# Kernel tuning notes

Measured on AMD Instinct MI355X. Metric: run time of the kernel, lower is better.

## Reference

```python
import jax, jax.numpy as jnp
import numpy as np
from jax import lax

B, S, H = 1, 2048, 1024
NH, NKV, HD = 16, 4, 64        # heads, kv heads, head_dim = H // NH
I = 3584                        # intermediate size
E, TOPK = 8, 2                  # experts, top-k routing
EPS = 1e-5
THETA = 1e6


def setup_inputs() -> dict:
    key = jax.random.key(0)
    ks = jax.random.split(key, 12)
    sc = 0.02
    return {
        "hidden_states": jax.random.normal(ks[0], (B, S, H), jnp.float32),
        "position_ids": jnp.broadcast_to(jnp.arange(S, dtype=jnp.int32), (B, S)),
        "wq": jax.random.normal(ks[1], (H, NH * HD), jnp.float32) * sc,
        "wk": jax.random.normal(ks[2], (H, NKV * HD), jnp.float32) * sc,
        "wv": jax.random.normal(ks[3], (H, NKV * HD), jnp.float32) * sc,
        "wo": jax.random.normal(ks[4], (NH * HD, H), jnp.float32) * sc,
        "input_norm_w": jnp.ones((H,), jnp.float32),
        "post_norm_w": jnp.ones((H,), jnp.float32),
        "gate_w": jax.random.normal(ks[5], (H, E), jnp.float32) * sc,
        "w1": jax.random.normal(ks[6], (E, H, I), jnp.float32) * sc,
        "w3": jax.random.normal(ks[7], (E, H, I), jnp.float32) * sc,
        "w2": jax.random.normal(ks[8], (E, I, H), jnp.float32) * sc,
    }


def _rmsnorm(x, w):
    var = jnp.mean(jnp.square(x), axis=-1, keepdims=True)
    return x * lax.rsqrt(var + EPS) * w


def _rope(q, k, position_ids):
    # q: [B,S,NH,HD], k: [B,S,NKV,HD]
    inv_freq = 1.0 / (THETA ** (jnp.arange(0, HD, 2, dtype=jnp.float32) / HD))
    freqs = position_ids.astype(jnp.float32)[..., None] * inv_freq  # [B,S,HD/2]
    emb = jnp.concatenate([freqs, freqs], axis=-1)                  # [B,S,HD]
    cos = jnp.cos(emb)[:, :, None, :]
    sin = jnp.sin(emb)[:, :, None, :]

    def rot_half(x):
        x1, x2 = jnp.split(x, 2, axis=-1)
        return jnp.concatenate([-x2, x1], axis=-1)

    return q * cos + rot_half(q) * sin, k * cos + rot_half(k) * sin


def _attention(x, position_ids, wq, wk, wv, wo):
    b, s, _ = x.shape
    q = (x @ wq).reshape(b, s, NH, HD)
    k = (x @ wk).reshape(b, s, NKV, HD)
    v = (x @ wv).reshape(b, s, NKV, HD)
    q, k = _rope(q, k, position_ids)
    groups = NH // NKV
    k = jnp.repeat(k, groups, axis=2)  # [B,S,NH,HD]
    v = jnp.repeat(v, groups, axis=2)
    scale = HD ** -0.5
    scores = jnp.einsum("bqhd,bkhd->bhqk", q, k) * scale
    causal = jnp.tril(jnp.ones((s, s), dtype=bool))
    scores = jnp.where(causal[None, None], scores, jnp.finfo(scores.dtype).min)
    probs = jax.nn.softmax(scores, axis=-1)
    out = jnp.einsum("bhqk,bkhd->bqhd", probs, v).reshape(b, s, NH * HD)
    return out @ wo


def _moe(x, gate_w, w1, w3, w2):
    b, s, h = x.shape
    xt = x.reshape(b * s, h)
    logits = xt @ gate_w                      # [T,E]
    probs = jax.nn.softmax(logits, axis=-1)
    top_w, top_i = lax.top_k(probs, TOPK)     # [T,K]
    top_w = top_w / jnp.sum(top_w, axis=-1, keepdims=True)
    out = jnp.zeros_like(xt)
    for e in range(E):
        we = jnp.sum(jnp.where(top_i == e, top_w, 0.0), axis=-1)   # [T]
        h_e = jax.nn.silu(xt @ w1[e]) * (xt @ w3[e])               # [T,I]
        out = out + we[:, None] * (h_e @ w2[e])
    return out.reshape(b, s, h), logits


def reference(hidden_states, position_ids, wq, wk, wv, wo,
              input_norm_w, post_norm_w, gate_w, w1, w3, w2):
    # MixtralDecoderLayer: norm -> GQA attn -> residual -> norm -> MoE -> residual
    attn_out = _attention(_rmsnorm(hidden_states, input_norm_w),
                          position_ids, wq, wk, wv, wo)
    h = hidden_states + attn_out
    moe_out, _router_logits = _moe(_rmsnorm(h, post_norm_w), gate_w, w1, w3, w2)
    return h + moe_out
```

## Files before the change

kernel.cpp:

```cpp
#include <hip/hip_runtime.h>
#include <math.h>


typedef unsigned short u16;
typedef unsigned int u32;
typedef __attribute__((ext_vector_type(8))) short s16x8;
typedef __attribute__((ext_vector_type(8))) _Float16 f16x8;
typedef __attribute__((ext_vector_type(4))) float f32x4;

#define S_LEN 2048
#define HDIM  1024
#define NHEAD 16
#define NKVH  4
#define HD    64
#define ISZ   3584
#define NEXP  8
#define NSLOT 4096
#define EPS_F 1e-5f
#define NEG_INF -1e30f
#define LOG2E 1.44269504f

__device__ __forceinline__ float bf2f(u16 u) {
    union { u32 i; float f; } c; c.i = ((u32)u) << 16; return c.f;
}
__device__ __forceinline__ u16 f2bf(float f) {
    union { float f; u32 i; } c; c.f = f;
    u32 r = (c.i + 0x7fffu + ((c.i >> 16) & 1u)) >> 16;
    return (u16)r;
}
__device__ __forceinline__ u16 f2h_bits(float f) {
    union { _Float16 h; u16 u; } c; c.h = (_Float16)f; return c.u;
}
__device__ __forceinline__ void async16(const u16* g, u16* l) {
    __builtin_amdgcn_global_load_lds(
        (const __attribute__((address_space(1))) void*)g,
        (__attribute__((address_space(3))) void*)l, 16, 0, 0);
}

__global__ void k_zero_ints(int* __restrict__ p, int n) {
    int i = blockIdx.x * blockDim.x + threadIdx.x;
    if (i < n) p[i] = 0;
}

__global__ __launch_bounds__(256)
void k_rmsnorm_bf(const float* __restrict__ x, const float* __restrict__ w,
                  u16* __restrict__ out) {
    int t = blockIdx.x;
    int tid = threadIdx.x;
    float4 v = ((const float4*)(x + (size_t)t * HDIM))[tid];
    float ss = v.x * v.x + v.y * v.y + v.z * v.z + v.w * v.w;
#pragma unroll
    for (int off = 32; off >= 1; off >>= 1) ss += __shfl_xor(ss, off, 64);
    __shared__ float red[4];
    if ((tid & 63) == 0) red[tid >> 6] = ss;
    __syncthreads();
    float tot = red[0] + red[1] + red[2] + red[3];
    float rstd = rsqrtf(tot * (1.0f / HDIM) + EPS_F);
    float4 wv = ((const float4*)w)[tid];
    uint2 pk;
    pk.x = (u32)f2bf(v.x * rstd * wv.x) | ((u32)f2bf(v.y * rstd * wv.y) << 16);
    pk.y = (u32)f2bf(v.z * rstd * wv.z) | ((u32)f2bf(v.w * rstd * wv.w) << 16);
    ((uint2*)(out + (size_t)t * HDIM))[tid] = pk;
}

__global__ __launch_bounds__(256)
void k_cvt_t(const float* __restrict__ src, u16* __restrict__ dst,
             int R, int C, long long srcZ, long long dstZ) {
    const int z = blockIdx.z;
    src += (size_t)z * srcZ;
    dst += (size_t)z * dstZ;
    const int lane = threadIdx.x & 63, w = threadIdx.x >> 6;
    const int c = blockIdx.x * 64 + lane;
    const int r0 = blockIdx.y * 128 + w * 32;
    float v[32];
#pragma unroll
    for (int i = 0; i < 32; i++) v[i] = src[(size_t)(r0 + i) * C + c];
#pragma unroll
    for (int g = 0; g < 4; g++) {
        uint4 pk;
        pk.x = (u32)f2bf(v[g * 8 + 0]) | ((u32)f2bf(v[g * 8 + 1]) << 16);
        pk.y = (u32)f2bf(v[g * 8 + 2]) | ((u32)f2bf(v[g * 8 + 3]) << 16);
        pk.z = (u32)f2bf(v[g * 8 + 4]) | ((u32)f2bf(v[g * 8 + 5]) << 16);
        pk.w = (u32)f2bf(v[g * 8 + 6]) | ((u32)f2bf(v[g * 8 + 7]) << 16);
        *(uint4*)(&dst[(size_t)c * R + r0 + g * 8]) = pk;
    }
}

__device__ __forceinline__ void stage32(const u16* __restrict__ A,
                                        const u16* __restrict__ Bt, int K,
                                        int rowA0, int rowAmax, int n0, int kc,
                                        u16* buf, int wid, int sr, int sc) {
#pragma unroll
    for (int t = 0; t < 2; t++) {
        int row = wid * 32 + t * 16 + sr;
        int ck = (sc ^ (row & 3)) << 3;
        int ra = rowA0 + row;
        if (ra > rowAmax) ra = rowAmax;
        u16* ldsA = buf + (wid * 32 + t * 16) * 32;
        async16(A + (size_t)ra * K + kc + ck, ldsA);
        async16(Bt + (size_t)(n0 + row) * K + kc + ck, ldsA + 4096);
    }
}

__device__ __forceinline__ void stage32_w13(const u16* __restrict__ A,
                                            const u16* __restrict__ B1,
                                            const u16* __restrict__ B3, int K,
                                            int rowA0, int rowAmax, int n0,
                                            int kc, u16* buf, int wid, int sr,
                                            int sc) {
#pragma unroll
    for (int t = 0; t < 2; t++) {
        int row = wid * 32 + t * 16 + sr;
        int ck = (sc ^ (row & 3)) << 3;
        int ra = rowA0 + row;
        if (ra > rowAmax) ra = rowAmax;
        u16* ldsA = buf + (wid * 32 + t * 16) * 32;
        async16(A + (size_t)ra * K + kc + ck, ldsA);
        async16(B1 + (size_t)(n0 + row) * K + kc + ck, ldsA + 4096);
        async16(B3 + (size_t)(n0 + row) * K + kc + ck, ldsA + 8192);
    }
}

__device__ __forceinline__ void gemm128_dbuf(
    const u16* __restrict__ A, const u16* __restrict__ Bt, int K,
    int kbeg, int kend, int rowA0, int rowAmax, int n0,
    u16* lds, f32x4 acc[4][4]) {
    const int tid = threadIdx.x;
    const int lane = tid & 63, wid = tid >> 6;
    const int sr = lane >> 2, sc = lane & 3;
    const int ln = lane & 15, q = lane >> 4;
    const int wm = wid >> 1, wn = wid & 1;
    stage32(A, Bt, K, rowA0, rowAmax, n0, kbeg, lds, wid, sr, sc);
    int pp = 0;
    for (int kc = kbeg; kc < kend; kc += 32) {
        u16* cur = lds + pp * 8192;
        u16* nxt = lds + (pp ^ 1) * 8192;
        pp ^= 1;
        __syncthreads();
        if (kc + 32 < kend)
            stage32(A, Bt, K, rowA0, rowAmax, n0, kc + 32, nxt, wid, sr, sc);
        s16x8 af[4], bfv[4];
#pragma unroll
        for (int i = 0; i < 4; i++) {
            int ar = wm * 64 + i * 16 + ln;
            af[i] = *(const s16x8*)(cur + ar * 32 + ((q ^ (ar & 3)) << 3));
            int br = wn * 64 + i * 16 + ln;
            bfv[i] = *(const s16x8*)(cur + 4096 + br * 32 + ((q ^ (br & 3)) << 3));
        }
#pragma unroll
        for (int i = 0; i < 4; i++)
#pragma unroll
            for (int j = 0; j < 4; j++)
                acc[i][j] = __builtin_amdgcn_mfma_f32_16x16x32_bf16(
                    af[i], bfv[j], acc[i][j], 0, 0, 0);
    }
}

__global__ __launch_bounds__(256, 2)
void k_gemm_bt(const u16* __restrict__ A, const u16* __restrict__ Bt,
               int M, int N, int K, int mode,
               float* __restrict__ F0, float* __restrict__ F1,
               const float* __restrict__ RES, u16* __restrict__ O16) {
    __shared__ u16 lds[16384];
    const int m0 = blockIdx.y * 128, n0 = blockIdx.x * 128;
    f32x4 acc[4][4];
#pragma unroll
    for (int i = 0; i < 4; i++)
#pragma unroll
        for (int j = 0; j < 4; j++) acc[i][j] = (f32x4){0.f, 0.f, 0.f, 0.f};
    gemm128_dbuf(A, Bt, K, 0, K, m0, M - 1, n0, lds, acc);
    const int lane = threadIdx.x & 63, wid = threadIdx.x >> 6;
    const int ln = lane & 15, q = lane >> 4, wm = wid >> 1, wn = wid & 1;
#pragma unroll
    for (int i = 0; i < 4; i++) {
#pragma unroll
        for (int r = 0; r < 4; r++) {
            int m = m0 + wm * 64 + i * 16 + q * 4 + r;
#pragma unroll
            for (int j = 0; j < 4; j++) {
                int n = n0 + wn * 64 + j * 16 + ln;
                float v = acc[i][j][r];
                if (mode == 0) {
                    F0[(size_t)m * N + n] = v;
                } else if (mode == 1) {
                    O16[(size_t)m * N + n] = f2bf(v);
                } else if (mode == 2) {
                    F0[(size_t)m * N + n] = v + RES[(size_t)m * N + n];
                } else {
                    if (n < 1024)       F0[(size_t)m * 1024 + n] = v;
                    else if (n < 1280)  F1[(size_t)m * 256 + (n - 1024)] = v;
                    else                O16[(size_t)m * 256 + (n - 1280)] = f2h_bits(v);
                }
            }
        }
    }
}

__global__ __launch_bounds__(256, 2)
void k_moe_w13(const u16* __restrict__ Xg, const u16* __restrict__ W1T,
               const u16* __restrict__ W3T, u16* __restrict__ He,
               const int* __restrict__ offs) {
    const int bid = blockIdx.x;
    const int xcd = bid & 7;
    const int r_ = bid >> 3;
    const int mb = r_ & 15;
    const int gslot = r_ >> 4;
    const int gid = gslot * 8 + xcd;
    const int e = gid / 28;
    const int nb = gid - e * 28;
    const int base = offs[e], cnt = offs[e + 1] - base;
    const int m0 = mb * 128;
    if (m0 >= cnt) return;
    __shared__ u16 lds[24576];
    const u16* B1 = W1T + (size_t)e * ISZ * HDIM;
    const u16* B3 = W3T + (size_t)e * ISZ * HDIM;
    const int n0 = nb * 128;
    f32x4 acc1[4][4], acc3[4][4];
#pragma unroll
    for (int i = 0; i < 4; i++)
#pragma unroll
        for (int j = 0; j < 4; j++) {
            acc1[i][j] = (f32x4){0.f, 0.f, 0.f, 0.f};
            acc3[i][j] = (f32x4){0.f, 0.f, 0.f, 0.f};
        }
    const int tid = threadIdx.x;
    const int lane = tid & 63, wid = tid >> 6;
    const int sr = lane >> 2, sc = lane & 3;
    const int ln = lane & 15, q = lane >> 4;
    const int wm = wid >> 1, wn = wid & 1;
    const int rowA0 = base + m0;
    stage32_w13(Xg, B1, B3, HDIM, rowA0, NSLOT - 1, n0, 0, lds, wid, sr, sc);
    int pp = 0;
    for (int kc = 0; kc < HDIM; kc += 32) {
        u16* cur = lds + pp * 12288;
        u16* nxt = lds + (pp ^ 1) * 12288;
        pp ^= 1;
        __syncthreads();
        if (kc + 32 < HDIM)
            stage32_w13(Xg, B1, B3, HDIM, rowA0, NSLOT - 1, n0, kc + 32, nxt,
                        wid, sr, sc);
        s16x8 af[4], b1f[4], b3f[4];
#pragma unroll
        for (int i = 0; i < 4; i++) {
            int ar = wm * 64 + i * 16 + ln;
            af[i] = *(const s16x8*)(cur + ar * 32 + ((q ^ (ar & 3)) << 3));
            int br = wn * 64 + i * 16 + ln;
            int bo = br * 32 + ((q ^ (br & 3)) << 3);
            b1f[i] = *(const s16x8*)(cur + 4096 + bo);
            b3f[i] = *(const s16x8*)(cur + 8192 + bo);
        }
#pragma unroll
        for (int i = 0; i < 4; i++)
#pragma unroll
            for (int j = 0; j < 4; j++) {
                acc1[i][j] = __builtin_amdgcn_mfma_f32_16x16x32_bf16(
                    af[i], b1f[j], acc1[i][j], 0, 0, 0);
                acc3[i][j] = __builtin_amdgcn_mfma_f32_16x16x32_bf16(
                    af[i], b3f[j], acc3[i][j], 0, 0, 0);
            }
    }
#pragma unroll
    for (int i = 0; i < 4; i++) {
#pragma unroll
        for (int r = 0; r < 4; r++) {
            int mloc = wm * 64 + i * 16 + q * 4 + r;
            if (m0 + mloc >= cnt) continue;
            size_t row = (size_t)(base + m0 + mloc);
#pragma unroll
            for (int j = 0; j < 4; j++) {
                int n = n0 + wn * 64 + j * 16 + ln;
                float v1 = acc1[i][j][r];
                float v3 = acc3[i][j][r];
                float s = v1 / (1.0f + expf(-v1));
                He[row * ISZ + n] = f2bf(s * v3);
            }
        }
    }
}

__global__ __launch_bounds__(256, 2)
void k_moe_w2(const u16* __restrict__ He, const u16* __restrict__ W2T,
              float* __restrict__ OA, float* __restrict__ OB,
              const int* __restrict__ offs) {
    const int z = blockIdx.z;
    const int e = z & 7, half = z >> 3;
    const int base = offs[e], cnt = offs[e + 1] - base;
    const int m0 = blockIdx.y * 128;
    if (m0 >= cnt) return;
    __shared__ u16 lds[16384];
    const u16* Bt = W2T + (size_t)e * HDIM * ISZ;
    const int n0 = blockIdx.x * 128;
    f32x4 acc[4][4];
#pragma unroll
    for (int i = 0; i < 4; i++)
#pragma unroll
        for (int j = 0; j < 4; j++) acc[i][j] = (f32x4){0.f, 0.f, 0.f, 0.f};
    gemm128_dbuf(He, Bt, ISZ, half * (ISZ / 2), (half + 1) * (ISZ / 2),
                 base + m0, NSLOT - 1, n0, lds, acc);
    float* F0 = half ? OB : OA;
    const int lane = threadIdx.x & 63, wid = threadIdx.x >> 6;
    const int ln = lane & 15, q = lane >> 4, wm = wid >> 1, wn = wid & 1;
#pragma unroll
    for (int i = 0; i < 4; i++) {
#pragma unroll
        for (int r = 0; r < 4; r++) {
            int mloc = wm * 64 + i * 16 + q * 4 + r;
            if (m0 + mloc >= cnt) continue;
            size_t row = (size_t)(base + m0 + mloc);
#pragma unroll
            for (int j = 0; j < 4; j++) {
                int n = n0 + wn * 64 + j * 16 + ln;
                F0[row * HDIM + n] = acc[i][j][r];
            }
        }
    }
}

__global__ __launch_bounds__(256)
void k_rope_cvt(const float* __restrict__ q, const float* __restrict__ k,
                const int* __restrict__ pos, u16* __restrict__ qb2,
                u16* __restrict__ kb2) {
    int id = blockIdx.x * blockDim.x + threadIdx.x;
    int d = id & 31;
    int hh = (id >> 5) % (NHEAD + NKVH);
    int s = id / ((NHEAD + NKVH) * 32);
    float p = (float)pos[s];
    float inv = exp2f(-((float)(2 * d) / (float)HD) * log2f(1.0e6f));
    float ang = p * inv;
    float c = cosf(ang), sn = sinf(ang);
    const float* sp; u16* dp;
    if (hh < NHEAD) {
        sp = q + (size_t)s * (NHEAD * HD) + hh * HD;
        dp = qb2 + (size_t)s * (NHEAD * HD) + hh * HD;
    } else {
        sp = k + (size_t)s * (NKVH * HD) + (hh - NHEAD) * HD;
        dp = kb2 + (size_t)s * (NKVH * HD) + (hh - NHEAD) * HD;
    }
    float x1 = sp[d], x2 = sp[d + 32];
    dp[d]      = f2h_bits(x1 * c - x2 * sn);
    dp[d + 32] = f2h_bits(x2 * c + x1 * sn);
}

__global__ __launch_bounds__(256)
void k_attn_mfma(const u16* __restrict__ qb, const u16* __restrict__ kb,
                 const u16* __restrict__ vb, u16* __restrict__ ob) {
    __shared__ u16 Qs[64 * 64];
    __shared__ u16 Ks[64 * 64];
    __shared__ u16 Vt[64 * 64];
    __shared__ u16 Ps[64 * 64];
    const int qt = blockIdx.x, h = blockIdx.y, kvh = h >> 2;
    const int tid = threadIdx.x, lane = tid & 63, w = tid >> 6;
    const int ln = lane & 15, quad = lane >> 4;

#pragma unroll
    for (int p = 0; p < 2; p++) {
        int r = p * 32 + (tid >> 3), c = tid & 7;
        uint4 v = *(const uint4*)(qb + (size_t)(qt * 64 + r) * (NHEAD * HD) +
                                  h * HD + c * 8);
        *(uint4*)&Qs[r * 64 + ((c ^ (r & 7)) << 3)] = v;
    }

    float m_[4], l_[4];
    f32x4 Oa[4];
#pragma unroll
    for (int r = 0; r < 4; r++) { m_[r] = NEG_INF; l_[r] = 0.0f; }
#pragma unroll
    for (int nt = 0; nt < 4; nt++) Oa[nt] = (f32x4){0.f, 0.f, 0.f, 0.f};

    for (int kt = 0; kt <= qt; kt++) {
        __syncthreads();
#pragma unroll
        for (int p = 0; p < 2; p++) {
            int r = p * 32 + (tid >> 3), c = tid & 7;
            uint4 v = *(const uint4*)(kb + (size_t)(kt * 64 + r) * (NKVH * HD) +
                                      kvh * HD + c * 8);
            *(uint4*)&Ks[r * 64 + ((c ^ (r & 7)) << 3)] = v;
        }
        {
            int s = tid & 63;
#pragma unroll
            for (int half = 0; half < 2; half++) {
                int d0 = w * 16 + half * 8;
                uint4 v = *(const uint4*)(vb + (size_t)(kt * 64 + s) * (NKVH * HD) +
                                          kvh * HD + d0);
                u16 a[8];
                a[0] = (u16)(v.x & 0xffff); a[1] = (u16)(v.x >> 16);
                a[2] = (u16)(v.y & 0xffff); a[3] = (u16)(v.y >> 16);
                a[4] = (u16)(v.z & 0xffff); a[5] = (u16)(v.z >> 16);
                a[6] = (u16)(v.w & 0xffff); a[7] = (u16)(v.w >> 16);
#pragma unroll
                for (int j = 0; j < 8; j++) {
                    int d = d0 + j;
                    Vt[d * 64 + (((s >> 3) ^ (d & 7)) << 3) + (s & 7)] = a[j];
                }
            }
        }
        __syncthreads();

        f32x4 sc[4];
#pragma unroll
        for (int nt = 0; nt < 4; nt++) sc[nt] = (f32x4){0.f, 0.f, 0.f, 0.f};
#pragma unroll
        for (int ks = 0; ks < 2; ks++) {
            int arow = 16 * w + ln;
            f16x8 af = *(const f16x8*)&Qs[arow * 64 +
                                          (((ks * 4 + quad) ^ (arow & 7)) << 3)];
#pragma unroll
            for (int nt = 0; nt < 4; nt++) {
                int brow = nt * 16 + ln;
                f16x8 bf = *(const f16x8*)&Ks[brow * 64 +
                                              (((ks * 4 + quad) ^ (brow & 7)) << 3)];
                sc[nt] = __builtin_amdgcn_mfma_f32_16x16x32_f16(af, bf, sc[nt],
                                                                0, 0, 0);
            }
        }

        const bool diag = (kt == qt);
        float mt[4];
#pragma unroll
        for (int r = 0; r < 4; r++) {
            int qrow = quad * 4 + r + 16 * w;
#pragma unroll
            for (int nt = 0; nt < 4; nt++) {
                float s = sc[nt][r] * 0.125f;
                if (diag && (nt * 16 + ln) > qrow) s = NEG_INF;
                sc[nt][r] = s;
            }
            mt[r] = fmaxf(fmaxf(sc[0][r], sc[1][r]), fmaxf(sc[2][r], sc[3][r]));
        }
#pragma unroll
        for (int off = 8; off >= 1; off >>= 1)
#pragma unroll
            for (int r = 0; r < 4; r++)
                mt[r] = fmaxf(mt[r], __shfl_xor(mt[r], off, 64));

        float rs[4];
#pragma unroll
        for (int r = 0; r < 4; r++) {
            float mn = fmaxf(m_[r], mt[r]);
            float al = exp2f((m_[r] - mn) * LOG2E);
            m_[r] = mn;
            float acc0 = 0.0f;
#pragma unroll
            for (int nt = 0; nt < 4; nt++) {
                float pv = exp2f((sc[nt][r] - mn) * LOG2E);
                sc[nt][r] = pv;
                acc0 += pv;
            }
            rs[r] = acc0;
            l_[r] *= al;
#pragma unroll
            for (int nt = 0; nt < 4; nt++) Oa[nt][r] *= al;
        }
#pragma unroll
        for (int off = 8; off >= 1; off >>= 1)
#pragma unroll
            for (int r = 0; r < 4; r++) rs[r] += __shfl_xor(rs[r], off, 64);
#pragma unroll
        for (int r = 0; r < 4; r++) l_[r] += rs[r];

#pragma unroll
        for (int r = 0; r < 4; r++) {
            int row = 16 * w + quad * 4 + r;
#pragma unroll
            for (int nt = 0; nt < 4; nt++) {
                int ch = nt * 2 + (ln >> 3);
                Ps[row * 64 + ((ch ^ (row & 7)) << 3) + (ln & 7)] =
                    f2h_bits(sc[nt][r]);
            }
        }
        __syncthreads();

#pragma unroll
        for (int ks = 0; ks < 2; ks++) {
            int arow = 16 * w + ln;
            f16x8 pf = *(const f16x8*)&Ps[arow * 64 +
                                          (((ks * 4 + quad) ^ (arow & 7)) << 3)];
#pragma unroll
            for (int nt = 0; nt < 4; nt++) {
                int vrow = nt * 16 + ln;
                f16x8 vf = *(const f16x8*)&Vt[vrow * 64 +
                                              (((ks * 4 + quad) ^ (vrow & 7)) << 3)];
                Oa[nt] = __builtin_amdgcn_mfma_f32_16x16x32_f16(pf, vf, Oa[nt],
                                                                0, 0, 0);
            }
        }
    }

#pragma unroll
    for (int r = 0; r < 4; r++) {
        float inv = 1.0f / l_[r];
        int sg = qt * 64 + 16 * w + quad * 4 + r;
#pragma unroll
        for (int nt = 0; nt < 4; nt++) {
            int d = nt * 16 + ln;
            ob[(size_t)sg * HDIM + h * HD + d] = f2bf(Oa[nt][r] * inv);
        }
    }
}

__global__ __launch_bounds__(64)
void k_gate(const float* __restrict__ Hst, const float* __restrict__ PW,
            const float* __restrict__ GW, int* __restrict__ cnt,
            int* __restrict__ top_i, float* __restrict__ top_w) {
    int t = blockIdx.x;
    int lane = threadIdx.x;
    const float* hrow = Hst + (size_t)t * HDIM;
    float ss = 0.0f;
    float acc[NEXP] = {};
    for (int hh = lane; hh < HDIM; hh += 64) {
        float hv = hrow[hh];
        ss += hv * hv;
        float xw = hv * PW[hh];
        const float* g = GW + (size_t)hh * NEXP;
#pragma unroll
        for (int e = 0; e < NEXP; e++) acc[e] += xw * g[e];
    }
#pragma unroll
    for (int off = 32; off >= 1; off >>= 1) {
        ss += __shfl_xor(ss, off, 64);
#pragma unroll
        for (int e = 0; e < NEXP; e++) acc[e] += __shfl_xor(acc[e], off, 64);
    }
    if (lane == 0) {
        float rstd = rsqrtf(ss * (1.0f / HDIM) + EPS_F);
        int e0 = 0;
        for (int e = 1; e < NEXP; e++) if (acc[e] > acc[e0]) e0 = e;
        int e1 = (e0 == 0) ? 1 : 0;
        for (int e = 0; e < NEXP; e++)
            if (e != e0 && acc[e] > acc[e1]) e1 = e;
        float w0 = 1.0f / (1.0f + expf((acc[e1] - acc[e0]) * rstd));
        top_i[t * 2 + 0] = e0; top_i[t * 2 + 1] = e1;
        top_w[t * 2 + 0] = w0; top_w[t * 2 + 1] = 1.0f - w0;
        atomicAdd(&cnt[e0], 1);
        atomicAdd(&cnt[e1], 1);
    }
}

__global__ void k_prefix(const int* __restrict__ cnt, int* __restrict__ offs,
                         int* __restrict__ cur) {
    if (blockIdx.x == 0 && threadIdx.x == 0) {
        int a = 0;
        for (int e = 0; e < NEXP; e++) { offs[e] = a; cur[e] = a; a += cnt[e]; }
        offs[NEXP] = a;
    }
}

__global__ __launch_bounds__(256)
void k_fill(const int* __restrict__ top_i, int* __restrict__ cur,
            int* __restrict__ idxg, int* __restrict__ slot) {
    int t = blockIdx.x * blockDim.x + threadIdx.x;
    if (t >= S_LEN) return;
#pragma unroll
    for (int kk = 0; kk < 2; kk++) {
        int e = top_i[t * 2 + kk];
        int p = atomicAdd(&cur[e], 1);
        idxg[p] = t;
        slot[t * 2 + kk] = p;
    }
}

__global__ __launch_bounds__(256)
void k_gather(const u16* __restrict__ xnb, const int* __restrict__ idxg,
              u16* __restrict__ Xg) {
    int p = blockIdx.x;
    int t = idxg[p];
    const uint2* s = (const uint2*)(xnb + (size_t)t * HDIM);
    uint2* d = (uint2*)(Xg + (size_t)p * HDIM);
    d[threadIdx.x] = s[threadIdx.x];
}

__global__ __launch_bounds__(256)
void k_combine2(const float* __restrict__ OA, const float* __restrict__ OB,
                const int* __restrict__ slot, const float* __restrict__ top_w,
                float* __restrict__ out) {
    int t = blockIdx.x, tid = threadIdx.x;
    int s0 = slot[t * 2], s1 = slot[t * 2 + 1];
    float w0 = top_w[t * 2], w1 = top_w[t * 2 + 1];
    float4 a0 = ((const float4*)(OA + (size_t)s0 * HDIM))[tid];
    float4 b0 = ((const float4*)(OB + (size_t)s0 * HDIM))[tid];
    float4 a1 = ((const float4*)(OA + (size_t)s1 * HDIM))[tid];
    float4 b1 = ((const float4*)(OB + (size_t)s1 * HDIM))[tid];
    float4* o = (float4*)(out + (size_t)t * HDIM);
    float4 c = o[tid];
    c.x += w0 * (a0.x + b0.x) + w1 * (a1.x + b1.x);
    c.y += w0 * (a0.y + b0.y) + w1 * (a1.y + b1.y);
    c.z += w0 * (a0.z + b0.z) + w1 * (a1.z + b1.z);
    c.w += w0 * (a0.w + b0.w) + w1 * (a1.w + b1.w);
    o[tid] = c;
}

extern "C" void kernel_launch(void* const* d_in, const int* in_sizes, int n_in,
                              void* d_out, int out_size, void* d_ws,
                              size_t ws_size, hipStream_t stream) {
    (void)in_sizes; (void)n_in; (void)out_size; (void)ws_size;
    const float* hidden = (const float*)d_in[0];
    const int*   pos    = (const int*)d_in[1];
    const float* wq     = (const float*)d_in[2];
    const float* wk     = (const float*)d_in[3];
    const float* wv     = (const float*)d_in[4];
    const float* wo     = (const float*)d_in[5];
    const float* innw   = (const float*)d_in[6];
    const float* postnw = (const float*)d_in[7];
    const float* gatew  = (const float*)d_in[8];
    const float* w1     = (const float*)d_in[9];
    const float* w3     = (const float*)d_in[10];
    const float* w2     = (const float*)d_in[11];
    float* out = (float*)d_out;

    u16* w1t  = (u16*)d_ws;
    u16* w3t  = w1t + (size_t)NEXP * ISZ * HDIM;
    u16* w2t  = w3t + (size_t)NEXP * ISZ * HDIM;
    u16* qkvt = w2t + (size_t)NEXP * ISZ * HDIM;
    u16* wot  = qkvt + (size_t)1536 * HDIM;
    u16* xnb  = wot + (size_t)HDIM * HDIM;
    float* qbuf = (float*)(xnb + (size_t)S_LEN * HDIM);
    float* kbuf = qbuf + (size_t)S_LEN * HDIM;
    u16* vb16   = (u16*)(kbuf + (size_t)S_LEN * NKVH * HD);
    u16* qb2    = vb16 + (size_t)S_LEN * NKVH * HD;
    u16* kb2    = qb2 + (size_t)S_LEN * HDIM;
    u16* attnb  = kb2 + (size_t)S_LEN * NKVH * HD;
    float* oexpA = qbuf;
    u16* Xg  = attnb + (size_t)S_LEN * HDIM;
    u16* hg3 = Xg + (size_t)NSLOT * HDIM;
    u16* he  = hg3 + (size_t)NSLOT * ISZ;
    float* oexpB = (float*)(he + (size_t)NSLOT * ISZ);
    int* ib  = (int*)(oexpB + (size_t)NSLOT * HDIM);
    int*   cnt   = ib;
    int*   offs  = ib + 16;
    int*   cur   = ib + 32;
    int*   top_i = ib + 64;
    int*   slot  = ib + 64 + 4096;
    int*   idxg  = ib + 64 + 8192;
    float* top_w = (float*)(ib + 64 + 12288);

    const long long HI = (long long)HDIM * ISZ;

    k_zero_ints<<<1, 64, 0, stream>>>(cnt, 64);
    k_rmsnorm_bf<<<S_LEN, 256, 0, stream>>>(hidden, innw, xnb);

    k_cvt_t<<<dim3(16, 8, 1), 256, 0, stream>>>(wq, qkvt, 1024, 1024, 0, 0);
    k_cvt_t<<<dim3(4, 8, 1), 256, 0, stream>>>(wk, qkvt + (size_t)1024 * 1024, 1024, 256, 0, 0);
    k_cvt_t<<<dim3(4, 8, 1), 256, 0, stream>>>(wv, qkvt + (size_t)1280 * 1024, 1024, 256, 0, 0);
    k_cvt_t<<<dim3(16, 8, 1), 256, 0, stream>>>(wo, wot, 1024, 1024, 0, 0);
    k_cvt_t<<<dim3(56, 8, NEXP), 256, 0, stream>>>(w1, w1t, 1024, 3584, HI, HI);
    k_cvt_t<<<dim3(56, 8, NEXP), 256, 0, stream>>>(w3, w3t, 1024, 3584, HI, HI);
    k_cvt_t<<<dim3(16, 28, NEXP), 256, 0, stream>>>(w2, w2t, 3584, 1024, HI, HI);

    k_gemm_bt<<<dim3(12, 16), 256, 0, stream>>>(xnb, qkvt, 2048, 1536, 1024, 3,
                                                qbuf, kbuf, nullptr, vb16);
    k_rope_cvt<<<(S_LEN * (NHEAD + NKVH) * 32) / 256, 256, 0, stream>>>(
        qbuf, kbuf, pos, qb2, kb2);
    k_attn_mfma<<<dim3(32, 16), 256, 0, stream>>>(qb2, kb2, vb16, attnb);
    k_gemm_bt<<<dim3(8, 16), 256, 0, stream>>>(attnb, wot, 2048, 1024, 1024, 2,
                                               out, nullptr, hidden, nullptr);
    k_rmsnorm_bf<<<S_LEN, 256, 0, stream>>>(out, postnw, xnb);
    k_gate<<<S_LEN, 64, 0, stream>>>(out, postnw, gatew, cnt, top_i, top_w);
    k_prefix<<<1, 1, 0, stream>>>(cnt, offs, cur);
    k_fill<<<S_LEN / 256, 256, 0, stream>>>(top_i, cur, idxg, slot);
    k_gather<<<NSLOT, 256, 0, stream>>>(xnb, idxg, Xg);

    k_moe_w13<<<dim3(28 * 16 * NEXP), 256, 0, stream>>>(Xg, w1t, w3t, he, offs);
    k_moe_w2<<<dim3(8, 16, 16), 256, 0, stream>>>(he, w2t, oexpA, oexpB, offs);
    k_combine2<<<S_LEN, 256, 0, stream>>>(oexpA, oexpB, slot, top_w, out);
}
```

Before: 883.4 us.

## Use persistent work-list scheduling for MoE expert GEMMs with 512-thread w13 blocks

k_prefix now writes a compact list of the (expert, m-block) tiles that actually exist. Both MoE GEMM kernels become persistent grid-stride loops over that list, so blocks are no longer launched only to exit early on empty tiles. k_moe_w13 moves to 512 threads (8 waves, each owning a 64x32 sub-tile) with a smaller per-wave accumulator, and occupancy targets are raised. In exchange it drops the previous XCD-aware block ordering and adds per-tile loop overhead and extra barriers.

```diff
diff --git a/kernel.cpp b/kernel.cpp
--- a/kernel.cpp
+++ b/kernel.cpp
@@ -102,23 +102,19 @@
     }
 }
 
-__device__ __forceinline__ void stage32_w13(const u16* __restrict__ A,
-                                            const u16* __restrict__ B1,
-                                            const u16* __restrict__ B3, int K,
-                                            int rowA0, int rowAmax, int n0,
-                                            int kc, u16* buf, int wid, int sr,
-                                            int sc) {
-#pragma unroll
-    for (int t = 0; t < 2; t++) {
-        int row = wid * 32 + t * 16 + sr;
-        int ck = (sc ^ (row & 3)) << 3;
-        int ra = rowA0 + row;
-        if (ra > rowAmax) ra = rowAmax;
-        u16* ldsA = buf + (wid * 32 + t * 16) * 32;
-        async16(A + (size_t)ra * K + kc + ck, ldsA);
-        async16(B1 + (size_t)(n0 + row) * K + kc + ck, ldsA + 4096);
-        async16(B3 + (size_t)(n0 + row) * K + kc + ck, ldsA + 8192);
-    }
+__device__ __forceinline__ void stage_w13(const u16* __restrict__ A,
+                                          const u16* __restrict__ B1,
+                                          const u16* __restrict__ B3,
+                                          int rowA0, int n0, int kc,
+                                          u16* buf, int wid, int sr, int sc) {
+    int row = wid * 16 + sr;
+    int ck = (sc ^ (row & 3)) << 3;
+    int ra = rowA0 + row;
+    if (ra > NSLOT - 1) ra = NSLOT - 1;
+    u16* dst = buf + (wid * 16) * 32;
+    async16(A  + (size_t)ra * HDIM + kc + ck, dst);
+    async16(B1 + (size_t)(n0 + row) * HDIM + kc + ck, dst + 4096);
+    async16(B3 + (size_t)(n0 + row) * HDIM + kc + ck, dst + 8192);
 }
 
 __device__ __forceinline__ void gemm128_dbuf(
@@ -196,121 +192,127 @@
     }
 }
 
-__global__ __launch_bounds__(256, 2)
+__global__ __launch_bounds__(512, 4)
 void k_moe_w13(const u16* __restrict__ Xg, const u16* __restrict__ W1T,
                const u16* __restrict__ W3T, u16* __restrict__ He,
-               const int* __restrict__ offs) {
-    const int bid = blockIdx.x;
-    const int xcd = bid & 7;
-    const int r_ = bid >> 3;
-    const int mb = r_ & 15;
-    const int gslot = r_ >> 4;
-    const int gid = gslot * 8 + xcd;
-    const int e = gid / 28;
-    const int nb = gid - e * 28;
-    const int base = offs[e], cnt = offs[e + 1] - base;
-    const int m0 = mb * 128;
-    if (m0 >= cnt) return;
+               const int* __restrict__ offs, const int* __restrict__ mlist,
+               const int* __restrict__ nitems) {
     __shared__ u16 lds[24576];
-    const u16* B1 = W1T + (size_t)e * ISZ * HDIM;
-    const u16* B3 = W3T + (size_t)e * ISZ * HDIM;
-    const int n0 = nb * 128;
-    f32x4 acc1[4][4], acc3[4][4];
-#pragma unroll
-    for (int i = 0; i < 4; i++)
-#pragma unroll
-        for (int j = 0; j < 4; j++) {
-            acc1[i][j] = (f32x4){0.f, 0.f, 0.f, 0.f};
-            acc3[i][j] = (f32x4){0.f, 0.f, 0.f, 0.f};
-        }
+    const int NB = ISZ / 128;
+    const int tot = nitems[0] * NB;
     const int tid = threadIdx.x;
     const int lane = tid & 63, wid = tid >> 6;
     const int sr = lane >> 2, sc = lane & 3;
     const int ln = lane & 15, q = lane >> 4;
-    const int wm = wid >> 1, wn = wid & 1;
-    const int rowA0 = base + m0;
-    stage32_w13(Xg, B1, B3, HDIM, rowA0, NSLOT - 1, n0, 0, lds, wid, sr, sc);
-    int pp = 0;
-    for (int kc = 0; kc < HDIM; kc += 32) {
-        u16* cur = lds + pp * 12288;
-        u16* nxt = lds + (pp ^ 1) * 12288;
-        pp ^= 1;
+    const int wm = wid >> 2, wn = wid & 3;
+    for (int it = blockIdx.x; it < tot; it += gridDim.x) {
+        const int mi = it / NB, nb = it - mi * NB;
+        const int em = mlist[mi];
+        const int e = em >> 8, mb = em & 255;
+        const int base = offs[e], cnt = offs[e + 1] - base;
+        const int m0 = mb * 128, n0 = nb * 128;
+        const int rowA0 = base + m0;
+        const u16* B1 = W1T + (size_t)e * ISZ * HDIM;
+        const u16* B3 = W3T + (size_t)e * ISZ * HDIM;
+        f32x4 acc1[4][2], acc3[4][2];
+#pragma unroll
+        for (int i = 0; i < 4; i++)
+#pragma unroll
+            for (int j = 0; j < 2; j++) {
+                acc1[i][j] = (f32x4){0.f, 0.f, 0.f, 0.f};
+                acc3[i][j] = (f32x4){0.f, 0.f, 0.f, 0.f};
+            }
         __syncthreads();
-        if (kc + 32 < HDIM)
-            stage32_w13(Xg, B1, B3, HDIM, rowA0, NSLOT - 1, n0, kc + 32, nxt,
-                        wid, sr, sc);
-        s16x8 af[4], b1f[4], b3f[4];
+        stage_w13(Xg, B1, B3, rowA0, n0, 0, lds, wid, sr, sc);
+        int pp = 0;
+        for (int kc = 0; kc < HDIM; kc += 32) {
+            u16* cur = lds + pp * 12288;
+            u16* nxt = lds + (pp ^ 1) * 12288;
+            pp ^= 1;
+            __syncthreads();
+            if (kc + 32 < HDIM)
+                stage_w13(Xg, B1, B3, rowA0, n0, kc + 32, nxt, wid, sr, sc);
+            s16x8 af[4], b1f[2], b3f[2];
+#pragma unroll
+            for (int i = 0; i < 4; i++) {
+                int ar = wm * 64 + i * 16 + ln;
+                af[i] = *(const s16x8*)(cur + ar * 32 + ((q ^ (ar & 3)) << 3));
+            }
+#pragma unroll
+            for (int j = 0; j < 2; j++) {
+                int br = wn * 32 + j * 16 + ln;
+                int bo = br * 32 + ((q ^ (br & 3)) << 3);
+                b1f[j] = *(const s16x8*)(cur + 4096 + bo);
+                b3f[j] = *(const s16x8*)(cur + 8192 + bo);
+            }
+#pragma unroll
+            for (int i = 0; i < 4; i++)
+#pragma unroll
+                for (int j = 0; j < 2; j++) {
+                    acc1[i][j] = __builtin_amdgcn_mfma_f32_16x16x32_bf16(
+                        af[i], b1f[j], acc1[i][j], 0, 0, 0);
+                    acc3[i][j] = __builtin_amdgcn_mfma_f32_16x16x32_bf16(
+                        af[i], b3f[j], acc3[i][j], 0, 0, 0);
+                }
+        }
 #pragma unroll
         for (int i = 0; i < 4; i++) {
-            int ar = wm * 64 + i * 16 + ln;
-            af[i] = *(const s16x8*)(cur + ar * 32 + ((q ^ (ar & 3)) << 3));
-            int br = wn * 64 + i * 16 + ln;
-            int bo = br * 32 + ((q ^ (br & 3)) << 3);
-            b1f[i] = *(const s16x8*)(cur + 4096 + bo);
-            b3f[i] = *(const s16x8*)(cur + 8192 + bo);
-        }
-#pragma unroll
-        for (int i = 0; i < 4; i++)
-#pragma unroll
-            for (int j = 0; j < 4; j++) {
-                acc1[i][j] = __builtin_amdgcn_mfma_f32_16x16x32_bf16(
-                    af[i], b1f[j], acc1[i][j], 0, 0, 0);
-                acc3[i][j] = __builtin_amdgcn_mfma_f32_16x16x32_bf16(
-                    af[i], b3f[j], acc3[i][j], 0, 0, 0);
-            }
-    }
-#pragma unroll
-    for (int i = 0; i < 4; i++) {
-#pragma unroll
-        for (int r = 0; r < 4; r++) {
-            int mloc = wm * 64 + i * 16 + q * 4 + r;
-            if (m0 + mloc >= cnt) continue;
-            size_t row = (size_t)(base + m0 + mloc);
-#pragma unroll
-            for (int j = 0; j < 4; j++) {
-                int n = n0 + wn * 64 + j * 16 + ln;
-                float v1 = acc1[i][j][r];
-                float v3 = acc3[i][j][r];
-                float s = v1 / (1.0f + expf(-v1));
-                He[row * ISZ + n] = f2bf(s * v3);
-            }
-        }
-    }
-}
-
-__global__ __launch_bounds__(256, 2)
+#pragma unroll
+            for (int r = 0; r < 4; r++) {
+                int mloc = wm * 64 + i * 16 + q * 4 + r;
+                if (m0 + mloc >= cnt) continue;
+                size_t row = (size_t)(base + m0 + mloc);
+#pragma unroll
+                for (int j = 0; j < 2; j++) {
+                    int n = n0 + wn * 32 + j * 16 + ln;
+                    float v1 = acc1[i][j][r];
+                    float v3 = acc3[i][j][r];
+                    float s = v1 / (1.0f + expf(-v1));
+                    He[row * ISZ + n] = f2bf(s * v3);
+                }
+            }
+        }
+    }
+}
+
+__global__ __launch_bounds__(256, 3)
 void k_moe_w2(const u16* __restrict__ He, const u16* __restrict__ W2T,
               float* __restrict__ OA, float* __restrict__ OB,
-              const int* __restrict__ offs) {
-    const int z = blockIdx.z;
-    const int e = z & 7, half = z >> 3;
-    const int base = offs[e], cnt = offs[e + 1] - base;
-    const int m0 = blockIdx.y * 128;
-    if (m0 >= cnt) return;
+              const int* __restrict__ offs, const int* __restrict__ mlist,
+              const int* __restrict__ nitems) {
     __shared__ u16 lds[16384];
-    const u16* Bt = W2T + (size_t)e * HDIM * ISZ;
-    const int n0 = blockIdx.x * 128;
-    f32x4 acc[4][4];
-#pragma unroll
-    for (int i = 0; i < 4; i++)
-#pragma unroll
-        for (int j = 0; j < 4; j++) acc[i][j] = (f32x4){0.f, 0.f, 0.f, 0.f};
-    gemm128_dbuf(He, Bt, ISZ, half * (ISZ / 2), (half + 1) * (ISZ / 2),
-                 base + m0, NSLOT - 1, n0, lds, acc);
-    float* F0 = half ? OB : OA;
+    const int tot = nitems[0] * 16;
     const int lane = threadIdx.x & 63, wid = threadIdx.x >> 6;
     const int ln = lane & 15, q = lane >> 4, wm = wid >> 1, wn = wid & 1;
-#pragma unroll
-    for (int i = 0; i < 4; i++) {
-#pragma unroll
-        for (int r = 0; r < 4; r++) {
-            int mloc = wm * 64 + i * 16 + q * 4 + r;
-            if (m0 + mloc >= cnt) continue;
-            size_t row = (size_t)(base + m0 + mloc);
-#pragma unroll
-            for (int j = 0; j < 4; j++) {
-                int n = n0 + wn * 64 + j * 16 + ln;
-                F0[row * HDIM + n] = acc[i][j][r];
+    for (int it = blockIdx.x; it < tot; it += gridDim.x) {
+        const int mi = it >> 4, rr = it & 15;
+        const int nb = rr & 7, half = rr >> 3;
+        const int em = mlist[mi];
+        const int e = em >> 8, mb = em & 255;
+        const int base = offs[e], cnt = offs[e + 1] - base;
+        const int m0 = mb * 128, n0 = nb * 128;
+        const u16* Bt = W2T + (size_t)e * HDIM * ISZ;
+        f32x4 acc[4][4];
+#pragma unroll
+        for (int i = 0; i < 4; i++)
+#pragma unroll
+            for (int j = 0; j < 4; j++) acc[i][j] = (f32x4){0.f, 0.f, 0.f, 0.f};
+        __syncthreads();
+        gemm128_dbuf(He, Bt, ISZ, half * (ISZ / 2), (half + 1) * (ISZ / 2),
+                     base + m0, NSLOT - 1, n0, lds, acc);
+        float* F0 = half ? OB : OA;
+#pragma unroll
+        for (int i = 0; i < 4; i++) {
+#pragma unroll
+            for (int r = 0; r < 4; r++) {
+                int mloc = wm * 64 + i * 16 + q * 4 + r;
+                if (m0 + mloc >= cnt) continue;
+                size_t row = (size_t)(base + m0 + mloc);
+#pragma unroll
+                for (int j = 0; j < 4; j++) {
+                    int n = n0 + wn * 64 + j * 16 + ln;
+                    F0[row * HDIM + n] = acc[i][j][r];
+                }
             }
         }
     }
@@ -538,11 +540,19 @@
 }
 
 __global__ void k_prefix(const int* __restrict__ cnt, int* __restrict__ offs,
-                         int* __restrict__ cur) {
+                         int* __restrict__ cur, int* __restrict__ mlist,
+                         int* __restrict__ nitems) {
     if (blockIdx.x == 0 && threadIdx.x == 0) {
-        int a = 0;
-        for (int e = 0; e < NEXP; e++) { offs[e] = a; cur[e] = a; a += cnt[e]; }
+        int a = 0, idx = 0;
+        for (int e = 0; e < NEXP; e++) {
+            offs[e] = a; cur[e] = a;
+            int c = cnt[e];
+            int nmb = (c + 127) >> 7;
+            for (int mb = 0; mb < nmb; mb++) mlist[idx++] = (e << 8) | mb;
+            a += c;
+        }
         offs[NEXP] = a;
+        nitems[0] = idx;
     }
 }
 
@@ -633,6 +643,8 @@
     int*   slot  = ib + 64 + 4096;
     int*   idxg  = ib + 64 + 8192;
     float* top_w = (float*)(ib + 64 + 12288);
+    int*   mlist = ib + 64 + 16384;
+    int*   nitems = ib + 64 + 16384 + 128;
 
     const long long HI = (long long)HDIM * ISZ;
 
@@ -656,11 +668,13 @@
                                                out, nullptr, hidden, nullptr);
     k_rmsnorm_bf<<<S_LEN, 256, 0, stream>>>(out, postnw, xnb);
     k_gate<<<S_LEN, 64, 0, stream>>>(out, postnw, gatew, cnt, top_i, top_w);
-    k_prefix<<<1, 1, 0, stream>>>(cnt, offs, cur);
+    k_prefix<<<1, 1, 0, stream>>>(cnt, offs, cur, mlist, nitems);
     k_fill<<<S_LEN / 256, 256, 0, stream>>>(top_i, cur, idxg, slot);
     k_gather<<<NSLOT, 256, 0, stream>>>(xnb, idxg, Xg);
 
-    k_moe_w13<<<dim3(28 * 16 * NEXP), 256, 0, stream>>>(Xg, w1t, w3t, he, offs);
-    k_moe_w2<<<dim3(8, 16, 16), 256, 0, stream>>>(he, w2t, oexpA, oexpB, offs);
+    k_moe_w13<<<dim3(512), 512, 0, stream>>>(Xg, w1t, w3t, he, offs, mlist,
+                                             nitems);
+    k_moe_w2<<<dim3(1024), 256, 0, stream>>>(he, w2t, oexpA, oexpB, offs,
+                                             mlist, nitems);
     k_combine2<<<S_LEN, 256, 0, stream>>>(oexpA, oexpB, slot, top_w, out);
 }
```

Measured after the change: 828.0 us. 6.3% less time.
